# Kernel tuning notes

Hardware: AMD Instinct MI355X
Metric: run time of the kernel (lower is better)

## Reference

```python
import jax, jax.numpy as jnp
import numpy as np

B, N, E, H, F, L, S = 4, 384, 768, 32, 3072, 12, 512
D = E // H


def setup_inputs() -> dict:
    key = jax.random.key(0)
    ks = jax.random.split(key, 32)
    inp = {}
    # forward args
    inp['node_type'] = jax.random.randint(ks[0], (B, N, 1), 1, S + 1)  # table has S+1 rows; 0 = pad (unused)
    inp['node_input_feature'] = jax.random.normal(ks[1], (B, N, E), jnp.float32)
    inp['in_degree'] = jax.random.randint(ks[2], (B, N), 0, S)
    inp['out_degree'] = jax.random.randint(ks[3], (B, N), 0, S)
    inp['attn_bias'] = jax.random.normal(ks[4], (B, N, N), jnp.float32) * 0.1
    inp['spatial_pos'] = jax.random.randint(ks[5], (B, N, N), 0, S)
    # embedding tables (normal stddev 0.02, as in the flax module)
    inp['node_emb'] = jax.random.normal(ks[6], (S + 1, E), jnp.float32) * 0.02
    inp['in_deg_emb'] = jax.random.normal(ks[7], (S, E), jnp.float32) * 0.02
    inp['out_deg_emb'] = jax.random.normal(ks[8], (S, E), jnp.float32) * 0.02
    inp['sp_emb'] = jax.random.normal(ks[9], (S, H), jnp.float32) * 0.02
    inp['sp_emb_rev'] = jax.random.normal(ks[10], (S, H), jnp.float32) * 0.02
    # per-layer weights, stacked along leading L axis
    se, sf = 1.0 / np.sqrt(E), 1.0 / np.sqrt(F)
    inp['Wq'] = jax.random.normal(ks[11], (L, E, E), jnp.float32) * se
    inp['bq'] = jax.random.normal(ks[12], (L, E), jnp.float32) * se
    inp['Wk'] = jax.random.normal(ks[13], (L, E, E), jnp.float32) * se
    inp['bk'] = jax.random.normal(ks[14], (L, E), jnp.float32) * se
    inp['Wv'] = jax.random.normal(ks[15], (L, E, E), jnp.float32) * se
    inp['bv'] = jax.random.normal(ks[16], (L, E), jnp.float32) * se
    inp['Wo'] = jax.random.normal(ks[17], (L, E, E), jnp.float32) * se
    inp['bo'] = jnp.zeros((L, E), jnp.float32)
    inp['W1'] = jax.random.normal(ks[18], (L, E, F), jnp.float32) * se
    inp['b1'] = jax.random.normal(ks[19], (L, F), jnp.float32) * se
    inp['W2'] = jax.random.normal(ks[20], (L, F, E), jnp.float32) * sf
    inp['b2'] = jax.random.normal(ks[21], (L, E), jnp.float32) * sf
    inp['ln1_s'] = jnp.ones((L, E), jnp.float32)
    inp['ln1_b'] = jnp.zeros((L, E), jnp.float32)
    inp['ln2_s'] = jnp.ones((L, E), jnp.float32)
    inp['ln2_b'] = jnp.zeros((L, E), jnp.float32)
    return inp


def _layernorm(x, scale, bias, eps=1e-5):
    m = x.mean(-1, keepdims=True)
    v = ((x - m) ** 2).mean(-1, keepdims=True)
    return (x - m) / jnp.sqrt(v + eps) * scale + bias


def _encoder(node_type, node_input_feature, in_degree, out_degree, attn_bias, spatial_pos,
             node_emb, in_deg_emb, out_deg_emb, sp_emb, sp_emb_rev,
             Wq, bq, Wk, bk, Wv, bv, Wo, bo, W1, b1, W2, b2, ln1_s, ln1_b, ln2_s, ln2_b):
    nt = node_type[..., 0]                               # [B,N]
    padding_mask = nt == 0                               # [B,N]
    # node features: node_emb(node_type).sum(-2) + degree embeddings + input feature
    x = (node_emb[node_type].sum(axis=-2)
         + in_deg_emb[in_degree] + out_deg_emb[out_degree]
         + node_input_feature)                           # [B,N,E]
    # spatial attention bias: [B,N,N,H] -> [B,H,N,N], plus graph-level attn_bias
    sb = sp_emb[spatial_pos] + sp_emb_rev[jnp.transpose(spatial_pos, (0, 2, 1))]
    bias = jnp.transpose(sb, (0, 3, 1, 2)) + attn_bias[:, None]  # [B,H,N,N]

    x = jnp.transpose(x, (1, 0, 2))                      # [N,B,E]
    scaling = D ** (-0.5)
    neg_inf = jnp.float32(-jnp.inf)

    def layer(x, p):
        wq, bq_, wk, bk_, wv, bv_, wo, bo_, w1, b1_, w2, b2_, s1, t1, s2, t2 = p
        q = ((x @ wq) + bq_) * scaling                   # [N,B,E], bias scaled too (faithful)
        k = (x @ wk) + bk_
        v = (x @ wv) + bv_
        q = q.reshape(N, B, H, D)
        k = k.reshape(N, B, H, D)
        v = v.reshape(N, B, H, D)
        w = jnp.einsum('nbhd,mbhd->bhnm', q, k) + bias   # [B,H,N,N]
        w = jnp.where(padding_mask[:, None, None, :], neg_inf, w)
        probs = jax.nn.softmax(w.astype(jnp.float32), axis=-1).astype(x.dtype)
        a = jnp.einsum('bhnm,mbhd->nbhd', probs, v).reshape(N, B, E)
        a = a @ wo + bo_
        x = _layernorm(x + a, s1, t1)                    # post-LN
        h = jax.nn.gelu(x @ w1 + b1_)                    # approximate gelu (flax default)
        h = h @ w2 + b2_
        x = _layernorm(x + h, s2, t2)
        return x, None

    xs = (Wq, bq, Wk, bk, Wv, bv, Wo, bo, W1, b1, W2, b2, ln1_s, ln1_b, ln2_s, ln2_b)
    x, _ = jax.lax.scan(layer, x, xs)
    return x                                             # [N,B,E]


def reference(node_type, node_input_feature, in_degree, out_degree, attn_bias, spatial_pos,
              node_emb, in_deg_emb, out_deg_emb, sp_emb, sp_emb_rev,
              Wq, bq, Wk, bk, Wv, bv, Wo, bo, W1, b1, W2, b2, ln1_s, ln1_b, ln2_s, ln2_b):
    return _encoder(node_type, node_input_feature, in_degree, out_degree, attn_bias, spatial_pos,
                    node_emb, in_deg_emb, out_deg_emb, sp_emb, sp_emb_rev,
                    Wq, bq, Wk, bk, Wv, bv, Wo, bo, W1, b1, W2, b2, ln1_s, ln1_b, ln2_s, ln2_b)
```

## Files before the change

kernel.cpp:

```cpp
#include <hip/hip_runtime.h>
#include <hip/hip_bf16.h>

#define Bb 4
#define Nn 384
#define Ee 768
#define Hh 32
#define Ff 3072
#define Ll 12
#define Ss 512
#define Mm (Nn*Bb)

typedef __attribute__((ext_vector_type(8))) short bf16x8;
typedef __attribute__((ext_vector_type(4))) float f32x4;
typedef unsigned short u16;

__device__ __forceinline__ u16 f2b(float f) {
  union { float f; unsigned int i; } c; c.f = f;
  unsigned int x = c.i;
  return (u16)((x + 0x7fffu + ((x >> 16) & 1u)) >> 16);
}
__device__ __forceinline__ float b2f(u16 u) {
  union { unsigned int i; float f; } c; c.i = ((unsigned int)u) << 16; return c.f;
}
__device__ __forceinline__ unsigned pkcvt(float lo, float hi) {
  unsigned r;
  asm("v_cvt_pk_bf16_f32 %0, %1, %2" : "=v"(r) : "v"(lo), "v"(hi));
  return r;
}
__device__ __forceinline__ void gload_lds16(const void* g, void* l) {
  __builtin_amdgcn_global_load_lds((__attribute__((address_space(1))) void*)(g),
                                   (__attribute__((address_space(3))) void*)(l), 16, 0, 0);
}

__global__ __launch_bounds__(256) void embed_kernel(
    const int* __restrict__ node_type, const float* __restrict__ nif,
    const int* __restrict__ in_deg, const int* __restrict__ out_deg,
    const float* __restrict__ node_emb, const float* __restrict__ ind_emb,
    const float* __restrict__ outd_emb,
    float* __restrict__ x, u16* __restrict__ xb)
{
  const int r = blockIdx.x;
  const int n = r / Bb, b = r % Bb;
  const int nt  = node_type[b*Nn + n];
  const int idg = in_deg[b*Nn + n];
  const int odg = out_deg[b*Nn + n];
  for (int c = threadIdx.x; c < Ee; c += 256) {
    float val = node_emb[(size_t)nt*Ee + c] + ind_emb[(size_t)idg*Ee + c]
              + outd_emb[(size_t)odg*Ee + c] + nif[((size_t)b*Nn + n)*Ee + c];
    x[(size_t)r*Ee + c] = val;
    xb[(size_t)r*Ee + c] = f2b(val);
  }
}

__global__ void spT_kernel(const int* __restrict__ sp, int* __restrict__ spT)
{
  __shared__ int tile[32][33];
  const int b = blockIdx.z;
  const int n0 = blockIdx.y * 32, m0 = blockIdx.x * 32;
  const int tx = threadIdx.x, ty = threadIdx.y;
  for (int i = ty; i < 32; i += 8)
    tile[i][tx] = sp[((size_t)b*Nn + n0 + i)*Nn + m0 + tx];
  __syncthreads();
  for (int i = ty; i < 32; i += 8)
    spT[((size_t)b*Nn + m0 + i)*Nn + n0 + tx] = tile[tx][i];
}

__global__ __launch_bounds__(256) void bias_pre_kernel(
    const float* __restrict__ atb, const int* __restrict__ sp, const int* __restrict__ spT,
    const float* __restrict__ sp_emb, const float* __restrict__ sp_emb_rev,
    u16* __restrict__ biasb)
{
  __shared__ float spc[512], sprc[512];
  const int bx = blockIdx.x, h = blockIdx.y, b = blockIdx.z;
  const int t = threadIdx.x;
  for (int i = t; i < 512; i += 256) {
    spc[i]  = sp_emb[(size_t)i*Hh + h];
    sprc[i] = sp_emb_rev[(size_t)i*Hh + h];
  }
  __syncthreads();
  const int qi = t >> 4;
  const int ml = (t & 15) << 2;
  const size_t rowb = ((size_t)b*Nn + bx*16 + qi)*Nn;
  u16* outb = biasb + ((size_t)(b*Hh + h)*24 + bx)*24*256;
  #pragma unroll
  for (int mg = 0; mg < 6; ++mg) {
    const int m = mg*64 + ml;
    float4 a4 = *(const float4*)(atb + rowb + m);
    int4  s4 = *(const int4*)(sp  + rowb + m);
    int4  t4 = *(const int4*)(spT + rowb + m);
    const int tt = m >> 4, hi2 = (m >> 2) & 3;
    uint2 u;
    u.x = pkcvt(a4.x + spc[s4.x] + sprc[t4.x], a4.y + spc[s4.y] + sprc[t4.y]);
    u.y = pkcvt(a4.z + spc[s4.z] + sprc[t4.z], a4.w + spc[s4.w] + sprc[t4.w]);
    *(uint2*)(outb + (tt >> 1)*512 + (hi2*16 + qi)*8 + (tt & 1)*4) = u;
  }
}

__global__ __launch_bounds__(256) void wconv_kernel(
    const float* __restrict__ Wq, const float* __restrict__ Wk, const float* __restrict__ Wv,
    const float* __restrict__ Wo, const float* __restrict__ W1, const float* __restrict__ W2,
    int layer, u16* __restrict__ slot)
{
  __shared__ float tile[64][65];
  int tid = blockIdx.x;
  const float* src; u16* dst; int Ns, Ks;
  if (tid < 432)       { int seg = tid / 144; tid -= seg*144;
                         src = (seg==0?Wq:(seg==1?Wk:Wv)) + (size_t)layer*Ee*Ee;
                         dst = slot + (size_t)seg*589824; Ns = 768; Ks = 768; }
  else if (tid < 576)  { tid -= 432; src = Wo + (size_t)layer*Ee*Ee; dst = slot + 1769472; Ns = 768;  Ks = 768; }
  else if (tid < 1152) { tid -= 576; src = W1 + (size_t)layer*Ee*Ff; dst = slot + 2359296; Ns = 3072; Ks = 768; }
  else                 { tid -= 1152; src = W2 + (size_t)layer*Ff*Ee; dst = slot + 4718592; Ns = 768; Ks = 3072; }
  const int tc = Ns >> 6;
  const int tk = tid / tc, tn = tid % tc;
  const int t = threadIdx.x;
  #pragma unroll
  for (int i = 0; i < 4; ++i) {
    const int id = t + i*256;
    const int r = id >> 4, c = (id & 15) << 2;
    float4 v = *(const float4*)(src + (size_t)(tk*64 + r)*Ns + tn*64 + c);
    tile[r][c+0] = v.x; tile[r][c+1] = v.y; tile[r][c+2] = v.z; tile[r][c+3] = v.w;
  }
  __syncthreads();
  #pragma unroll
  for (int i = 0; i < 2; ++i) {
    const int ch = t + i*256;
    const int n = ch >> 3, kc = (ch & 7) << 3;
    uint4 u;
    u.x = pkcvt(tile[kc+0][n], tile[kc+1][n]);
    u.y = pkcvt(tile[kc+2][n], tile[kc+3][n]);
    u.z = pkcvt(tile[kc+4][n], tile[kc+5][n]);
    u.w = pkcvt(tile[kc+6][n], tile[kc+7][n]);
    *(uint4*)(dst + (size_t)(tn*64 + n)*Ks + tk*64 + kc) = u;
  }
}

template<int EPI>
__global__ __launch_bounds__(256) void gemm3_kernel(
    const u16* __restrict__ A, const u16* __restrict__ Bw,
    const float* __restrict__ b0, const float* __restrict__ b1, const float* __restrict__ b2,
    int Kfull, int Kc, float scaleQ,
    float* __restrict__ outF, u16* __restrict__ outB)
{
  __shared__ __align__(16) u16 As[2][128][64];
  __shared__ __align__(16) u16 Bs[2][64][64];
  const int t = threadIdx.x, lane = t & 63, wave = t >> 6;
  int bx = blockIdx.x, by = blockIdx.y;
  {
    const int gx = gridDim.x;
    const int nwg = gx * gridDim.y;
    const int bid = bx + gx * by;
    const int cpx = nwg >> 3;
    const int s = (bid & 7) * cpx + (bid >> 3);
    bx = s % gx; by = s / gx;
  }
  const int m0 = bx * 128, n0 = by * 64;
  const int k0 = blockIdx.z * Kc;
  const int wm = wave >> 1, wn = wave & 1;
  const int ql = lane & 15, hi = lane >> 4;
  const int nk = Kc >> 6;
  const int sr = t >> 3;
  const int sslot = (t & 7) ^ (sr & 7);
  const size_t aoff = (size_t)(m0 + sr)*Kfull + k0 + (sslot << 3);
  const size_t boff = (size_t)(n0 + sr)*Kfull + k0 + (sslot << 3);
  const size_t rstep = (size_t)32 * Kfull;

  int aro[4][2], bro[2][2];
  #pragma unroll
  for (int ks = 0; ks < 2; ++ks) {
    const int kb = (((ks<<2) + hi) ^ (ql & 7)) << 4;
    #pragma unroll
    for (int f = 0; f < 4; ++f) aro[f][ks] = (wm*64 + f*16 + ql)*128 + kb;
    #pragma unroll
    for (int f = 0; f < 2; ++f) bro[f][ks] = (wn*32 + f*16 + ql)*128 + kb;
  }

  f32x4 acc[4][2];
  #pragma unroll
  for (int a = 0; a < 4; ++a)
    #pragma unroll
    for (int c = 0; c < 2; ++c) acc[a][c] = (f32x4){0.f,0.f,0.f,0.f};

  #pragma unroll
  for (int i = 0; i < 4; ++i)
    gload_lds16(A + aoff + i*rstep, (char*)&As[0][0][0] + i*4096 + t*16);
  #pragma unroll
  for (int i = 0; i < 2; ++i)
    gload_lds16(Bw + boff + i*rstep, (char*)&Bs[0][0][0] + i*4096 + t*16);

  for (int kt = 0; kt < nk; ++kt) {
    const int cur = kt & 1, nxt = cur ^ 1;
    const bool pre = (kt + 1 < nk);
    if (pre) {
      const size_t kk = (size_t)(kt + 1) << 6;
      #pragma unroll
      for (int i = 0; i < 4; ++i)
        gload_lds16(A + aoff + kk + i*rstep, (char*)&As[nxt][0][0] + i*4096 + t*16);
      #pragma unroll
      for (int i = 0; i < 2; ++i)
        gload_lds16(Bw + boff + kk + i*rstep, (char*)&Bs[nxt][0][0] + i*4096 + t*16);
      asm volatile("s_waitcnt vmcnt(6)" ::: "memory");
    } else {
      asm volatile("s_waitcnt vmcnt(0)" ::: "memory");
    }
    __builtin_amdgcn_s_barrier();
    __builtin_amdgcn_sched_barrier(0);

    const char* aBase = (const char*)&As[cur][0][0];
    const char* bBase = (const char*)&Bs[cur][0][0];
    bf16x8 af[4][2], bf[2][2];
    #pragma unroll
    for (int f = 0; f < 4; ++f)
      #pragma unroll
      for (int ks = 0; ks < 2; ++ks)
        af[f][ks] = *(const bf16x8*)(aBase + aro[f][ks]);
    #pragma unroll
    for (int f = 0; f < 2; ++f)
      #pragma unroll
      for (int ks = 0; ks < 2; ++ks)
        bf[f][ks] = *(const bf16x8*)(bBase + bro[f][ks]);
    #pragma unroll
    for (int ks = 0; ks < 2; ++ks)
      #pragma unroll
      for (int fm = 0; fm < 4; ++fm)
        #pragma unroll
        for (int fn = 0; fn < 2; ++fn)
          acc[fm][fn] = __builtin_amdgcn_mfma_f32_16x16x32_bf16(af[fm][ks], bf[fn][ks], acc[fm][fn], 0, 0, 0);
    if (pre) {
      __builtin_amdgcn_sched_barrier(0);
      __builtin_amdgcn_s_barrier();
    }
  }

  #pragma unroll
  for (int fm = 0; fm < 4; ++fm) {
    const int rowb = m0 + wm*64 + fm*16 + hi*4;
    #pragma unroll
    for (int fn = 0; fn < 2; ++fn) {
      const int gcol = n0 + wn*32 + fn*16 + ql;
      float bv, scale = 1.0f;
      if (EPI == 0) {
        const int seg = gcol / 768;
        const int cw = gcol - seg*768;
        bv = (seg == 0) ? b0[cw] : ((seg == 1) ? b1[cw] : b2[cw]);
        if (seg == 0) scale = scaleQ;
      } else if (EPI == 1) {
        bv = (blockIdx.z == 0) ? b0[gcol] : 0.0f;
      } else {
        bv = b0[gcol];
      }
      f32x4 v = acc[fm][fn];
      #pragma unroll
      for (int j = 0; j < 4; ++j) {
        float val = (v[j] + bv) * scale;
        if (EPI == 0) {
          outB[(size_t)(rowb + j) * 2304 + gcol] = f2b(val);
        } else if (EPI == 1) {
          outF[(size_t)blockIdx.z * (Mm*768) + (size_t)(rowb + j) * 768 + gcol] = val;
        } else {
          float arg = 0.7978845608028654f * (val + 0.044715f * val * val * val);
          float e = __expf(2.0f * arg);
          float g = 0.5f * val * (2.0f - 2.0f / (e + 1.0f));
          outB[(size_t)(rowb + j) * 3072 + gcol] = f2b(g);
        }
      }
    }
  }
}

template<int PREBIAS>
__global__ __launch_bounds__(256) void attn2_kernel(
    const u16* __restrict__ qkv,
    const u16* __restrict__ biasb,
    const float* __restrict__ atb, const int* __restrict__ sp, const int* __restrict__ spT,
    const float* __restrict__ sp_emb, const float* __restrict__ sp_emb_rev,
    u16* __restrict__ ab)
{
  __shared__ __align__(16) u16 Kt[384][32];
  __shared__ __align__(16) u16 Vt[32][392];
  __shared__ __align__(16) u16 Qt[128][32];
  __shared__ __align__(16) u16 Pw[4][16][32];
  __shared__ float spc[512], sprc[512];
  const int bid = blockIdx.x;
  const int pair = bid % 3;
  const int h = (bid / 3) % Hh;
  const int b = bid / (3 * Hh);
  const int t = threadIdx.x, lane = t & 63, wave = t >> 6;
  const int ql = lane & 15, hi = lane >> 4;

  for (int idx = t; idx < 384*3; idx += 256) {
    const int m = idx / 3, c = idx - m*3;
    const u16* base = qkv + ((size_t)m*Bb + b)*2304 + h*24 + c*8;
    uint4 kk = *(const uint4*)(base + 768);
    uint4 vv = *(const uint4*)(base + 1536);
    *(uint4*)&Kt[m][c*8] = kk;
    Vt[c*8+0][m] = (u16)(vv.x & 0xffffu); Vt[c*8+1][m] = (u16)(vv.x >> 16);
    Vt[c*8+2][m] = (u16)(vv.y & 0xffffu); Vt[c*8+3][m] = (u16)(vv.y >> 16);
    Vt[c*8+4][m] = (u16)(vv.z & 0xffffu); Vt[c*8+5][m] = (u16)(vv.z >> 16);
    Vt[c*8+6][m] = (u16)(vv.w & 0xffffu); Vt[c*8+7][m] = (u16)(vv.w >> 16);
  }
  for (int idx = t; idx < 384*2; idx += 256)
    *(uint2*)&Kt[idx>>1][24 + (idx&1)*4] = make_uint2(0u, 0u);
  for (int idx = t; idx < 8*196; idx += 256)
    *(unsigned*)((char*)&Vt[24][0] + idx*4) = 0u;
  for (int idx = t; idx < 128*3; idx += 256) {
    const int qr = idx / 3, c = idx - qr*3;
    const u16* base = qkv + ((size_t)(pair*128 + qr)*Bb + b)*2304 + h*24 + c*8;
    *(uint4*)&Qt[qr][c*8] = *(const uint4*)base;
  }
  for (int idx = t; idx < 128*2; idx += 256)
    *(uint2*)&Qt[idx>>1][24 + (idx&1)*4] = make_uint2(0u, 0u);
  if (!PREBIAS) {
    for (int i = t; i < 512; i += 256) {
      spc[i]  = sp_emb[(size_t)i*Hh + h];
      sprc[i] = sp_emb_rev[(size_t)i*Hh + h];
    }
  }
  __syncthreads();

  for (int qi = 0; qi < 2; ++qi) {
    const int ntile = pair*2 + qi;
    const int q0 = ntile*64 + wave*16;
    const int q = q0 + ql;
    const bf16x8 qf = *(const bf16x8*)&Qt[qi*64 + wave*16 + ql][hi*8];

    f32x4 f[24];
    const size_t crow = ((size_t)b*Nn + q)*Nn;
    if (PREBIAS) {
      const u16* bp = biasb + (((size_t)(b*Hh + h)*24 + ntile*4 + wave)*24)*256 + lane*8;
      #pragma unroll
      for (int tt2 = 0; tt2 < 12; ++tt2) {
        uint4 bb = *(const uint4*)(bp + tt2*512);
        {
          bf16x8 kf = *(const bf16x8*)&Kt[(2*tt2)*16 + ql][hi*8];
          f32x4 z = (f32x4){0.f,0.f,0.f,0.f};
          f32x4 s = __builtin_amdgcn_mfma_f32_16x16x32_bf16(kf, qf, z, 0, 0, 0);
          s[0] += b2f((u16)(bb.x & 0xffffu)); s[1] += b2f((u16)(bb.x >> 16));
          s[2] += b2f((u16)(bb.y & 0xffffu)); s[3] += b2f((u16)(bb.y >> 16));
          f[2*tt2] = s;
        }
        {
          bf16x8 kf = *(const bf16x8*)&Kt[(2*tt2+1)*16 + ql][hi*8];
          f32x4 z = (f32x4){0.f,0.f,0.f,0.f};
          f32x4 s = __builtin_amdgcn_mfma_f32_16x16x32_bf16(kf, qf, z, 0, 0, 0);
          s[0] += b2f((u16)(bb.z & 0xffffu)); s[1] += b2f((u16)(bb.z >> 16));
          s[2] += b2f((u16)(bb.w & 0xffffu)); s[3] += b2f((u16)(bb.w >> 16));
          f[2*tt2+1] = s;
        }
      }
    } else {
      #pragma unroll
      for (int tt = 0; tt < 24; ++tt) {
        bf16x8 kf = *(const bf16x8*)&Kt[tt*16 + ql][hi*8];
        f32x4 z = (f32x4){0.f,0.f,0.f,0.f};
        f32x4 s = __builtin_amdgcn_mfma_f32_16x16x32_bf16(kf, qf, z, 0, 0, 0);
        const int off = tt*16 + hi*4;
        int4 s4 = *(const int4*)(sp + crow + off);
        int4 t4 = *(const int4*)(spT + crow + off);
        float4 a4 = *(const float4*)(atb + crow + off);
        s[0] += a4.x + spc[s4.x] + sprc[t4.x];
        s[1] += a4.y + spc[s4.y] + sprc[t4.y];
        s[2] += a4.z + spc[s4.z] + sprc[t4.z];
        s[3] += a4.w + spc[s4.w] + sprc[t4.w];
        f[tt] = s;
      }
    }

    float mx = -3.0e38f;
    #pragma unroll
    for (int tt = 0; tt < 24; ++tt)
      mx = fmaxf(mx, fmaxf(fmaxf(f[tt][0], f[tt][1]), fmaxf(f[tt][2], f[tt][3])));
    mx = fmaxf(mx, __shfl_xor(mx, 16, 64));
    mx = fmaxf(mx, __shfl_xor(mx, 32, 64));
    float sum = 0.f;
    #pragma unroll
    for (int tt = 0; tt < 24; ++tt) {
      #pragma unroll
      for (int j = 0; j < 4; ++j) { f[tt][j] = __expf(f[tt][j] - mx); sum += f[tt][j]; }
    }
    sum += __shfl_xor(sum, 16, 64);
    sum += __shfl_xor(sum, 32, 64);
    const float inv = 1.0f / sum;

    f32x4 o0 = (f32x4){0.f,0.f,0.f,0.f}, o1 = (f32x4){0.f,0.f,0.f,0.f};
    char* prow = (char*)&Pw[wave][ql][0];
    const int swz = (ql & 3) << 4;
    #pragma unroll
    for (int c = 0; c < 12; ++c) {
      unsigned w0 = pkcvt(f[2*c][0],   f[2*c][1]);
      unsigned w1 = pkcvt(f[2*c][2],   f[2*c][3]);
      unsigned w2 = pkcvt(f[2*c+1][0], f[2*c+1][1]);
      unsigned w3 = pkcvt(f[2*c+1][2], f[2*c+1][3]);
      *(unsigned*)(prow + (((hi*8)      ) ^ swz)) = w0;
      *(unsigned*)(prow + (((hi*8) +  4) ^ swz)) = w1;
      *(unsigned*)(prow + (((hi*8) + 32) ^ swz)) = w2;
      *(unsigned*)(prow + (((hi*8) + 36) ^ swz)) = w3;
      bf16x8 a = *(const bf16x8*)(prow + ((hi*16) ^ swz));
      bf16x8 v0 = *(const bf16x8*)&Vt[ql][c*32 + hi*8];
      bf16x8 v1 = *(const bf16x8*)&Vt[16 + ql][c*32 + hi*8];
      o0 = __builtin_amdgcn_mfma_f32_16x16x32_bf16(a, v0, o0, 0, 0, 0);
      o1 = __builtin_amdgcn_mfma_f32_16x16x32_bf16(a, v1, o1, 0, 0, 0);
    }

    #pragma unroll
    for (int j = 0; j < 4; ++j) {
      float invj = __shfl(inv, hi*4 + j, 64);
      const int qg = q0 + hi*4 + j;
      u16* orow = ab + ((size_t)qg*Bb + b)*Ee + h*24;
      orow[ql] = f2b(o0[j] * invj);
      if (ql < 8) orow[16 + ql] = f2b(o1[j] * invj);
    }
  }
}

template<int NP>
__global__ __launch_bounds__(256) void ln_kernel(
    const float* __restrict__ xin, const float* __restrict__ delta,
    const float* __restrict__ gamma, const float* __restrict__ beta,
    float* __restrict__ xout, u16* __restrict__ xb)
{
  const int wave = threadIdx.x >> 6, lane = threadIdx.x & 63;
  const int r = blockIdx.x * 4 + wave;
  const size_t base = (size_t)r * Ee;
  const int c0 = lane * 12;
  float v[12];
  #pragma unroll
  for (int i = 0; i < 3; ++i) {
    float4 xv = *(const float4*)(xin + base + c0 + i*4);
    v[i*4+0] = xv.x; v[i*4+1] = xv.y; v[i*4+2] = xv.z; v[i*4+3] = xv.w;
  }
  #pragma unroll
  for (int p = 0; p < NP; ++p) {
    const float* dp = delta + (size_t)p*(Mm*768) + base + c0;
    #pragma unroll
    for (int i = 0; i < 3; ++i) {
      float4 dv = *(const float4*)(dp + i*4);
      v[i*4+0] += dv.x; v[i*4+1] += dv.y; v[i*4+2] += dv.z; v[i*4+3] += dv.w;
    }
  }
  float s = 0.f;
  #pragma unroll
  for (int i = 0; i < 12; ++i) s += v[i];
  #pragma unroll
  for (int off = 1; off < 64; off <<= 1) s += __shfl_xor(s, off, 64);
  const float mean = s * (1.0f / 768.0f);
  float qs = 0.f;
  #pragma unroll
  for (int i = 0; i < 12; ++i) { float d = v[i] - mean; qs += d * d; }
  #pragma unroll
  for (int off = 1; off < 64; off <<= 1) qs += __shfl_xor(qs, off, 64);
  const float rstd = rsqrtf(qs * (1.0f / 768.0f) + 1e-5f);
  float o[12];
  #pragma unroll
  for (int i = 0; i < 3; ++i) {
    float4 g4 = *(const float4*)(gamma + c0 + i*4);
    float4 b4 = *(const float4*)(beta + c0 + i*4);
    o[i*4+0] = (v[i*4+0] - mean) * rstd * g4.x + b4.x;
    o[i*4+1] = (v[i*4+1] - mean) * rstd * g4.y + b4.y;
    o[i*4+2] = (v[i*4+2] - mean) * rstd * g4.z + b4.z;
    o[i*4+3] = (v[i*4+3] - mean) * rstd * g4.w + b4.w;
    *(float4*)(xout + base + c0 + i*4) = make_float4(o[i*4+0], o[i*4+1], o[i*4+2], o[i*4+3]);
  }
  #pragma unroll
  for (int i = 0; i < 3; ++i) {
    uint2 u;
    u.x = pkcvt(o[i*4+0], o[i*4+1]);
    u.y = pkcvt(o[i*4+2], o[i*4+3]);
    *(uint2*)(xb + base + c0 + i*4) = u;
  }
}

extern "C" void kernel_launch(void* const* d_in, const int* in_sizes, int n_in,
                              void* d_out, int out_size, void* d_ws, size_t ws_size,
                              hipStream_t stream) {
  const int*   node_type  = (const int*)d_in[0];
  const float* nif        = (const float*)d_in[1];
  const int*   in_deg     = (const int*)d_in[2];
  const int*   out_deg    = (const int*)d_in[3];
  const float* atb        = (const float*)d_in[4];
  const int*   sp         = (const int*)d_in[5];
  const float* node_emb   = (const float*)d_in[6];
  const float* ind_emb    = (const float*)d_in[7];
  const float* outd_emb   = (const float*)d_in[8];
  const float* sp_emb     = (const float*)d_in[9];
  const float* sp_emb_rev = (const float*)d_in[10];
  const float* Wq = (const float*)d_in[11]; const float* bq = (const float*)d_in[12];
  const float* Wk = (const float*)d_in[13]; const float* bk = (const float*)d_in[14];
  const float* Wv = (const float*)d_in[15]; const float* bv = (const float*)d_in[16];
  const float* Wo = (const float*)d_in[17]; const float* bo = (const float*)d_in[18];
  const float* W1 = (const float*)d_in[19]; const float* b1 = (const float*)d_in[20];
  const float* W2 = (const float*)d_in[21]; const float* b2 = (const float*)d_in[22];
  const float* ln1s = (const float*)d_in[23]; const float* ln1b = (const float*)d_in[24];
  const float* ln2s = (const float*)d_in[25]; const float* ln2b = (const float*)d_in[26];

  char* ws = (char*)d_ws;
  float* x      = (float*)(ws);
  u16*   xb     = (u16*)(ws +  4718592);
  u16*   qkvb16 = (u16*)(ws +  7077888);
  u16*   abuf   = (u16*)(ws + 14155776);
  u16*   hb     = (u16*)(ws + 16515072);
  float* obufP  = (float*)(ws + 25952256);
  int*   spTb   = (int*)(ws + 44826624);
  u16*   biasb  = (u16*)(ws + 47185920);
  u16*   wTslot = (u16*)(ws + 84934656);
  const bool useBias = ws_size >= 99090432ull;

  embed_kernel<<<Mm, 256, 0, stream>>>(node_type, nif, in_deg, out_deg,
                                       node_emb, ind_emb, outd_emb, x, xb);
  spT_kernel<<<dim3(12, 12, 4), dim3(32, 8), 0, stream>>>(sp, spTb);
  if (useBias)
    bias_pre_kernel<<<dim3(24, 32, 4), 256, 0, stream>>>(atb, sp, spTb, sp_emb, sp_emb_rev, biasb);

  const float scaleQ = 0.2041241452319315f;

  for (int l = 0; l < Ll; ++l) {
    const float *bql = bq + (size_t)l*Ee, *bkl = bk + (size_t)l*Ee, *bvl = bv + (size_t)l*Ee;
    const float *bol = bo + (size_t)l*Ee;
    const float *b1l = b1 + (size_t)l*Ff, *b2l = b2 + (size_t)l*Ee;

    wconv_kernel<<<1728, 256, 0, stream>>>(Wq, Wk, Wv, Wo, W1, W2, l, wTslot);
    const u16* qkvT = wTslot;
    const u16* woT  = wTslot + 1769472;
    const u16* w1T  = wTslot + 2359296;
    const u16* w2T  = wTslot + 4718592;

    gemm3_kernel<0><<<dim3(12, 36), 256, 0, stream>>>(xb, qkvT, bql, bkl, bvl,
                                                      768, 768, scaleQ, nullptr, qkvb16);
    if (useBias)
      attn2_kernel<1><<<384, 256, 0, stream>>>(qkvb16, biasb, atb, sp, spTb,
                                               sp_emb, sp_emb_rev, abuf);
    else
      attn2_kernel<0><<<384, 256, 0, stream>>>(qkvb16, nullptr, atb, sp, spTb,
                                               sp_emb, sp_emb_rev, abuf);
    gemm3_kernel<1><<<dim3(12, 12, 2), 256, 0, stream>>>(abuf, woT, bol, bol, bol,
                                                         768, 384, 1.0f, obufP, nullptr);
    ln_kernel<2><<<Mm/4, 256, 0, stream>>>(x, obufP, ln1s + (size_t)l*Ee, ln1b + (size_t)l*Ee, x, xb);
    gemm3_kernel<2><<<dim3(12, 48), 256, 0, stream>>>(xb, w1T, b1l, b1l, b1l,
                                                      768, 768, 1.0f, nullptr, hb);
    gemm3_kernel<1><<<dim3(12, 12, 4), 256, 0, stream>>>(hb, w2T, b2l, b2l, b2l,
                                                         3072, 768, 1.0f, obufP, nullptr);
    float* xdst = (l == Ll - 1) ? (float*)d_out : x;
    ln_kernel<4><<<Mm/4, 256, 0, stream>>>(x, obufP, ln2s + (size_t)l*Ee, ln2b + (size_t)l*Ee, xdst, xb);
  }
}
```

Before: 1.282 ms.

## Double-buffer weight slots and fuse next-layer weight conversion into FFN2 GEMM launch

Weight transpose/bf16 conversion for layer l+1 now runs inside the same launch as the layer-l FFN2 GEMM, with extra blocks, writing into an alternate weight slot. Layer 0 is converted up front. The aim is to hide the per-layer conversion traffic behind GEMM work and drop one kernel launch per layer. In exchange it needs a second weight slot, which raises the workspace threshold for the precomputed-bias path. The conversion blocks also now carry the GEMM's larger shared-memory allocation, which can lower their occupancy.

Measured after the change: 1.185 ms. 1.08x faster.

```diff
diff --git a/kernel.cpp b/kernel.cpp
--- a/kernel.cpp
+++ b/kernel.cpp
@@ -96,13 +96,12 @@
   }
 }
 
-__global__ __launch_bounds__(256) void wconv_kernel(
-    const float* __restrict__ Wq, const float* __restrict__ Wk, const float* __restrict__ Wv,
-    const float* __restrict__ Wo, const float* __restrict__ W1, const float* __restrict__ W2,
-    int layer, u16* __restrict__ slot)
-{
-  __shared__ float tile[64][65];
-  int tid = blockIdx.x;
+__device__ __forceinline__ void wconv_body(
+    int tid, int layer, char* smemRaw,
+    const float* Wq, const float* Wk, const float* Wv,
+    const float* Wo, const float* W1, const float* W2, u16* slot)
+{
+  float (*tile)[65] = (float(*)[65])smemRaw;
   const float* src; u16* dst; int Ns, Ks;
   if (tid < 432)       { int seg = tid / 144; tid -= seg*144;
                          src = (seg==0?Wq:(seg==1?Wk:Wv)) + (size_t)layer*Ee*Ee;
@@ -134,27 +133,35 @@
   }
 }
 
+__global__ __launch_bounds__(256) void wconv_kernel(
+    const float* __restrict__ Wq, const float* __restrict__ Wk, const float* __restrict__ Wv,
+    const float* __restrict__ Wo, const float* __restrict__ W1, const float* __restrict__ W2,
+    int layer, u16* __restrict__ slot)
+{
+  __shared__ __align__(16) char smem[16640];
+  wconv_body(blockIdx.x, layer, smem, Wq, Wk, Wv, Wo, W1, W2, slot);
+}
+
 template<int EPI>
-__global__ __launch_bounds__(256) void gemm3_kernel(
+__device__ __forceinline__ void gemm_body(
+    char* smemRaw, int bx0, int by0, int gx, int nwg, int zz,
     const u16* __restrict__ A, const u16* __restrict__ Bw,
     const float* __restrict__ b0, const float* __restrict__ b1, const float* __restrict__ b2,
     int Kfull, int Kc, float scaleQ,
     float* __restrict__ outF, u16* __restrict__ outB)
 {
-  __shared__ __align__(16) u16 As[2][128][64];
-  __shared__ __align__(16) u16 Bs[2][64][64];
+  u16 (*As)[128][64] = (u16(*)[128][64])smemRaw;
+  u16 (*Bs)[64][64]  = (u16(*)[64][64])(smemRaw + 32768);
   const int t = threadIdx.x, lane = t & 63, wave = t >> 6;
-  int bx = blockIdx.x, by = blockIdx.y;
+  int bx = bx0, by = by0;
   {
-    const int gx = gridDim.x;
-    const int nwg = gx * gridDim.y;
     const int bid = bx + gx * by;
     const int cpx = nwg >> 3;
     const int s = (bid & 7) * cpx + (bid >> 3);
     bx = s % gx; by = s / gx;
   }
   const int m0 = bx * 128, n0 = by * 64;
-  const int k0 = blockIdx.z * Kc;
+  const int k0 = zz * Kc;
   const int wm = wave >> 1, wn = wave & 1;
   const int ql = lane & 15, hi = lane >> 4;
   const int nk = Kc >> 6;
@@ -244,7 +251,7 @@
         bv = (seg == 0) ? b0[cw] : ((seg == 1) ? b1[cw] : b2[cw]);
         if (seg == 0) scale = scaleQ;
       } else if (EPI == 1) {
-        bv = (blockIdx.z == 0) ? b0[gcol] : 0.0f;
+        bv = (zz == 0) ? b0[gcol] : 0.0f;
       } else {
         bv = b0[gcol];
       }
@@ -255,7 +262,7 @@
         if (EPI == 0) {
           outB[(size_t)(rowb + j) * 2304 + gcol] = f2b(val);
         } else if (EPI == 1) {
-          outF[(size_t)blockIdx.z * (Mm*768) + (size_t)(rowb + j) * 768 + gcol] = val;
+          outF[(size_t)zz * (Mm*768) + (size_t)(rowb + j) * 768 + gcol] = val;
         } else {
           float arg = 0.7978845608028654f * (val + 0.044715f * val * val * val);
           float e = __expf(2.0f * arg);
@@ -264,6 +271,36 @@
         }
       }
     }
+  }
+}
+
+template<int EPI>
+__global__ __launch_bounds__(256) void gemm3_kernel(
+    const u16* __restrict__ A, const u16* __restrict__ Bw,
+    const float* __restrict__ b0, const float* __restrict__ b1, const float* __restrict__ b2,
+    int Kfull, int Kc, float scaleQ,
+    float* __restrict__ outF, u16* __restrict__ outB)
+{
+  __shared__ __align__(16) char smem[49152];
+  gemm_body<EPI>(smem, blockIdx.x, blockIdx.y, gridDim.x, gridDim.x*gridDim.y,
+                 blockIdx.z, A, Bw, b0, b1, b2, Kfull, Kc, scaleQ, outF, outB);
+}
+
+__global__ __launch_bounds__(256) void ffn2w_kernel(
+    const u16* __restrict__ A, const u16* __restrict__ w2T,
+    const float* __restrict__ b2v, float* __restrict__ outF,
+    const float* __restrict__ Wq, const float* __restrict__ Wk, const float* __restrict__ Wv,
+    const float* __restrict__ Wo, const float* __restrict__ W1, const float* __restrict__ W2,
+    int layerNext, u16* __restrict__ slotNext, int doW)
+{
+  __shared__ __align__(16) char smem[49152];
+  const int bid = blockIdx.x;
+  if (bid < 576) {
+    const int zz = bid / 144, r = bid - zz*144;
+    gemm_body<1>(smem, r % 12, r / 12, 12, 144, zz,
+                 A, w2T, b2v, b2v, b2v, 3072, 768, 1.0f, outF, nullptr);
+  } else if (doW) {
+    wconv_body(bid - 576, layerNext, smem, Wq, Wk, Wv, Wo, W1, W2, slotNext);
   }
 }
 
@@ -501,14 +538,17 @@
   float* obufP  = (float*)(ws + 25952256);
   int*   spTb   = (int*)(ws + 44826624);
   u16*   biasb  = (u16*)(ws + 47185920);
-  u16*   wTslot = (u16*)(ws + 84934656);
-  const bool useBias = ws_size >= 99090432ull;
+  u16*   wTs0   = (u16*)(ws + 84934656);
+  u16*   wTs1   = (u16*)(ws + 99090432);
+  const bool useBias = ws_size >= 113246208ull;
+  u16* slots[2] = { wTs0, wTs1 };
 
   embed_kernel<<<Mm, 256, 0, stream>>>(node_type, nif, in_deg, out_deg,
                                        node_emb, ind_emb, outd_emb, x, xb);
   spT_kernel<<<dim3(12, 12, 4), dim3(32, 8), 0, stream>>>(sp, spTb);
   if (useBias)
     bias_pre_kernel<<<dim3(24, 32, 4), 256, 0, stream>>>(atb, sp, spTb, sp_emb, sp_emb_rev, biasb);
+  wconv_kernel<<<1728, 256, 0, stream>>>(Wq, Wk, Wv, Wo, W1, W2, 0, slots[0]);
 
   const float scaleQ = 0.2041241452319315f;
 
@@ -517,11 +557,12 @@
     const float *bol = bo + (size_t)l*Ee;
     const float *b1l = b1 + (size_t)l*Ff, *b2l = b2 + (size_t)l*Ee;
 
-    wconv_kernel<<<1728, 256, 0, stream>>>(Wq, Wk, Wv, Wo, W1, W2, l, wTslot);
-    const u16* qkvT = wTslot;
-    const u16* woT  = wTslot + 1769472;
-    const u16* w1T  = wTslot + 2359296;
-    const u16* w2T  = wTslot + 4718592;
+    u16* slot = slots[l & 1];
+    u16* slotN = slots[(l + 1) & 1];
+    const u16* qkvT = slot;
+    const u16* woT  = slot + 1769472;
+    const u16* w1T  = slot + 2359296;
+    const u16* w2T  = slot + 4718592;
 
     gemm3_kernel<0><<<dim3(12, 36), 256, 0, stream>>>(xb, qkvT, bql, bkl, bvl,
                                                       768, 768, scaleQ, nullptr, qkvb16);
@@ -536,8 +577,9 @@
     ln_kernel<2><<<Mm/4, 256, 0, stream>>>(x, obufP, ln1s + (size_t)l*Ee, ln1b + (size_t)l*Ee, x, xb);
     gemm3_kernel<2><<<dim3(12, 48), 256, 0, stream>>>(xb, w1T, b1l, b1l, b1l,
                                                       768, 768, 1.0f, nullptr, hb);
-    gemm3_kernel<1><<<dim3(12, 12, 4), 256, 0, stream>>>(hb, w2T, b2l, b2l, b2l,
-                                                         3072, 768, 1.0f, obufP, nullptr);
+    ffn2w_kernel<<<2304, 256, 0, stream>>>(hb, w2T, b2l, obufP,
+                                           Wq, Wk, Wv, Wo, W1, W2,
+                                           l + 1, slotN, (l + 1 < Ll) ? 1 : 0);
     float* xdst = (l == Ll - 1) ? (float*)d_out : x;
     ln_kernel<4><<<Mm/4, 256, 0, stream>>>(x, obufP, ln2s + (size_t)l*Ee, ln2b + (size_t)l*Ee, xdst, xb);
   }
```
